# Kernel tuning notes

Measured on AMD Instinct MI355X. Metric: run time of the kernel, lower is better.

## Reference

```python
import jax, jax.numpy as jnp
import numpy as np


def setup_inputs() -> dict:
    key = jax.random.key(0)
    ks = jax.random.split(key, 5)
    S, B, I, H = 512, 64, 256, 1024
    scale_x = 1.0 / np.sqrt(I)
    scale_h = 1.0 / np.sqrt(H)
    return {
        "x": jax.random.normal(ks[0], (S, B, I), dtype=jnp.float32),
        "Wx": jax.random.normal(ks[1], (H, I), dtype=jnp.float32) * scale_x,
        "bx": jax.random.normal(ks[2], (H,), dtype=jnp.float32) * scale_x,
        "Wh": jax.random.normal(ks[3], (H, H), dtype=jnp.float32) * scale_h,
        "bh": jax.random.normal(ks[4], (H,), dtype=jnp.float32) * scale_h,
    }


def reference(x, Wx, bx, Wh, bh):
    # x: (S, B, I). Vanilla RNN: h_t = tanh(Wh h_{t-1} + bh + Wx x_t + bx)
    S, B, I = x.shape
    H = Wh.shape[0]
    # Precompute input projections for all timesteps in one big GEMM.
    xproj = jnp.einsum("sbi,hi->sbh", x, Wx) + bx  # (S, B, H)

    def step(h, xp_t):
        h_new = jnp.tanh(h @ Wh.T + bh + xp_t)  # (B, H)
        return h_new, h_new

    h0 = jnp.zeros((B, H), dtype=x.dtype)
    h_last, h_seq = jax.lax.scan(step, h0, xproj)
    return h_seq, h_last[None]  # (S,B,H), (1,B,H)
```

## Files before the change

kernel.cpp:

```cpp
#include <hip/hip_runtime.h>
#include <cstddef>

#define S_ 512
#define B_ 64
#define I_ 256
#define H_ 1024

#define NG 8
#define GB 8
#define JT 32
#define GBLK 32

__global__ __launch_bounds__(256) void transpose_k(const float* __restrict__ in,
                                                   float* __restrict__ out,
                                                   int R, int C) {
  __shared__ float t[32][33];
  int c0 = blockIdx.x * 32, r0 = blockIdx.y * 32;
  int x = threadIdx.x & 31, y = threadIdx.x >> 5;
  for (int i = 0; i < 32; i += 8) {
    t[y + i][x] = in[(size_t)(r0 + y + i) * C + (c0 + x)];
  }
  __syncthreads();
  for (int i = 0; i < 32; i += 8) {
    out[(size_t)(c0 + y + i) * R + (r0 + x)] = t[x][y + i];
  }
}

__global__ __launch_bounds__(256) void xproj_kernel(const float* __restrict__ x,
                                                    const float* __restrict__ WxT,
                                                    const float* __restrict__ bx,
                                                    float* __restrict__ out) {
  __shared__ float xs[8][I_];
  int tid = threadIdx.x;
  int j = blockIdx.x * 256 + tid;
  size_t m0 = (size_t)blockIdx.y * 8;
  const float* xrow = x + m0 * I_;
  #pragma unroll
  for (int r = 0; r < 8; ++r) xs[r][tid] = xrow[(size_t)r * I_ + tid];
  __syncthreads();

  float bj = bx[j];
  float a[8];
  #pragma unroll
  for (int r = 0; r < 8; ++r) a[r] = bj;
  const float* wp = WxT + j;
  for (int k = 0; k < I_; k += 4) {
    float w0 = wp[(size_t)(k + 0) * H_];
    float w1 = wp[(size_t)(k + 1) * H_];
    float w2 = wp[(size_t)(k + 2) * H_];
    float w3 = wp[(size_t)(k + 3) * H_];
    #pragma unroll
    for (int r = 0; r < 8; ++r) {
      float4 v = *(const float4*)&xs[r][k];
      a[r] += w0 * v.x + w1 * v.y + w2 * v.z + w3 * v.w;
    }
  }
  #pragma unroll
  for (int r = 0; r < 8; ++r) out[(m0 + r) * H_ + j] = a[r];
}

__global__ __launch_bounds__(512, 2) void rnn_persistent(
    const float* __restrict__ Wh, const float* __restrict__ bh,
    float* __restrict__ out, unsigned* __restrict__ flags) {
  __shared__ float4 Hs4[GB * 256];

  const int tid = threadIdx.x;
  const int g  = blockIdx.x & 7;
  const int jt = blockIdx.x >> 3;
  const int j0 = jt * JT, b0 = g * GB;
  const int jj = tid >> 4;
  const int ks = tid & 15;
  const int ksw = ks & 7;

  float4 Wreg[16];
  {
    const float4* wp = (const float4*)(Wh + (size_t)(j0 + jj) * H_) + ks * 16;
    #pragma unroll
    for (int i = 0; i < 16; ++i) Wreg[i] = wp[i];
  }
  const float bh_j = bh[j0 + jj];
  const size_t oidx = (size_t)(b0 + ksw) * H_ + (size_t)(j0 + jj);
  float* const out_last = out + (size_t)S_ * B_ * H_;
  unsigned* const flagg = flags + (size_t)g * GBLK;

  for (int t = 0; t < S_; ++t) {
    float* orow = out + (size_t)t * B_ * H_;
    float xv = orow[oidx];

    float s = 0.f;
    if (t > 0) {
      const float* hsrc =
          (const float*)(out + (size_t)(t - 1) * B_ * H_ + (size_t)b0 * H_);
      float4 hv[4];
      #pragma unroll
      for (int q = 0; q < 4; ++q) {
        const float* ap = hsrc + (size_t)(q * 512 + tid) * 4;
        asm volatile("global_load_dwordx4 %0, %1, off sc1"
                     : "=v"(hv[q]) : "v"(ap));
      }
      asm volatile("s_waitcnt vmcnt(0)" ::: "memory");
      __builtin_amdgcn_sched_barrier(0);
      #pragma unroll
      for (int q = 0; q < 4; ++q) {
        int f = q * 512 + tid;
        Hs4[f ^ ((f >> 4) & 7)] = hv[q];
      }
      __syncthreads();

      float acc[8] = {0.f, 0.f, 0.f, 0.f, 0.f, 0.f, 0.f, 0.f};
      const int kb = ks * 16;
      #pragma unroll
      for (int i = 0; i < 16; ++i) {
        const int l0 = kb + (i ^ ksw);
        const float4 w = Wreg[i];
        #pragma unroll
        for (int b = 0; b < 8; ++b) {
          float4 h = Hs4[b * 256 + l0];
          acc[b] += w.x * h.x + w.y * h.y + w.z * h.z + w.w * h.w;
        }
      }
      #pragma unroll
      for (int b = 0; b < 8; ++b) {
        float v = acc[b];
        v += __shfl_xor(v, 1, 64);
        v += __shfl_xor(v, 2, 64);
        v += __shfl_xor(v, 4, 64);
        v += __shfl_xor(v, 8, 64);
        acc[b] = v;
      }
      float sv = acc[0];
      #pragma unroll
      for (int b = 1; b < 8; ++b) sv = (ks == b) ? acc[b] : sv;
      s = sv;
    }

    if (ks < GB) {
      float hval = tanhf(s + bh_j + xv);
      if (t == S_ - 1) out_last[oidx] = hval;
      __hip_atomic_store(&orow[oidx], hval, __ATOMIC_RELAXED,
                         __HIP_MEMORY_SCOPE_AGENT);
    }

    if (t < S_ - 1) {
      asm volatile("s_waitcnt vmcnt(0)" ::: "memory");
      __syncthreads();
      if (tid == 0) {
        __hip_atomic_store(&flagg[jt], (unsigned)(t + 1), __ATOMIC_RELAXED,
                           __HIP_MEMORY_SCOPE_AGENT);
      }
      if (tid < 64) {
        unsigned* fp = &flagg[tid & 31];
        const unsigned tgt = (unsigned)(t + 1);
        while (__hip_atomic_load(fp, __ATOMIC_RELAXED,
                                 __HIP_MEMORY_SCOPE_AGENT) < tgt)
          __builtin_amdgcn_s_sleep(1);
      }
      __syncthreads();
    }
  }
}

extern "C" void kernel_launch(void* const* d_in, const int* in_sizes, int n_in,
                              void* d_out, int out_size, void* d_ws, size_t ws_size,
                              hipStream_t stream) {
  const float* x  = (const float*)d_in[0];
  const float* Wx = (const float*)d_in[1];
  const float* bx = (const float*)d_in[2];
  const float* Wh = (const float*)d_in[3];
  const float* bh = (const float*)d_in[4];
  float* out = (float*)d_out;
  float* WxT = (float*)d_ws;
  unsigned* flags = (unsigned*)(WxT + (size_t)I_ * H_);

  (void)hipMemsetAsync(flags, 0, NG * GBLK * sizeof(unsigned), stream);
  hipLaunchKernelGGL(transpose_k, dim3(I_ / 32, H_ / 32), dim3(256), 0, stream,
                     Wx, WxT, H_, I_);
  hipLaunchKernelGGL(xproj_kernel, dim3(H_ / 256, (S_ * B_) / 8), dim3(256), 0, stream,
                     x, WxT, bx, out);

  void* args[] = {(void*)&Wh, (void*)&bh, (void*)&out, (void*)&flags};
  hipError_t e = hipLaunchCooperativeKernel((const void*)rnn_persistent,
                                            dim3(256), dim3(512), args, 0, stream);
  if (e != hipSuccess) {
    hipLaunchKernelGGL(rnn_persistent, dim3(256), dim3(512), 0, stream,
                       Wh, bh, out, flags);
  }
}
```

Baseline: 4.300 ms.

## Interleave two batch groups per block to overlap barrier waits with compute

```diff
diff --git a/kernel.cpp b/kernel.cpp
--- a/kernel.cpp
+++ b/kernel.cpp
@@ -8,8 +8,8 @@
 
 #define NG 8
 #define GB 8
-#define JT 32
-#define GBLK 32
+#define JT 16
+#define GBLK 64
 
 __global__ __launch_bounds__(256) void transpose_k(const float* __restrict__ in,
                                                    float* __restrict__ out,
@@ -65,97 +65,177 @@
   __shared__ float4 Hs4[GB * 256];
 
   const int tid = threadIdx.x;
-  const int g  = blockIdx.x & 7;
-  const int jt = blockIdx.x >> 3;
-  const int j0 = jt * JT, b0 = g * GB;
-  const int jj = tid >> 4;
-  const int ks = tid & 15;
-  const int ksw = ks & 7;
-
-  float4 Wreg[16];
+  const int pr = blockIdx.x & 3;
+  const int jt = blockIdx.x >> 2;
+  const int j0 = jt * JT;
+  const int b0A = pr * GB, b0B = (pr + 4) * GB;
+  const int jj = tid >> 5;
+  const int ks = tid & 31;
+  const int hsw = (ks >> 1) & 7;
+
+  float4 Wreg[8];
   {
-    const float4* wp = (const float4*)(Wh + (size_t)(j0 + jj) * H_) + ks * 16;
+    const float4* wp = (const float4*)(Wh + (size_t)(j0 + jj) * H_) + ks * 8;
     #pragma unroll
-    for (int i = 0; i < 16; ++i) Wreg[i] = wp[i];
+    for (int i = 0; i < 8; ++i) {
+      const float4* ap = wp + i;
+      asm volatile("global_load_dwordx4 %0, %1, off" : "=v"(Wreg[i]) : "v"(ap));
+    }
+    asm volatile("s_waitcnt vmcnt(0)" ::: "memory");
+    __builtin_amdgcn_sched_barrier(0);
   }
   const float bh_j = bh[j0 + jj];
-  const size_t oidx = (size_t)(b0 + ksw) * H_ + (size_t)(j0 + jj);
+  const size_t oidxA = (size_t)(b0A + (ks & 7)) * H_ + (size_t)(j0 + jj);
+  const size_t oidxB = (size_t)(b0B + (ks & 7)) * H_ + (size_t)(j0 + jj);
   float* const out_last = out + (size_t)S_ * B_ * H_;
-  unsigned* const flagg = flags + (size_t)g * GBLK;
+  unsigned* const flagsA = flags + (size_t)pr * GBLK;
+  unsigned* const flagsB = flags + (size_t)(pr + 4) * GBLK;
 
   for (int t = 0; t < S_; ++t) {
     float* orow = out + (size_t)t * B_ * H_;
-    float xv = orow[oidx];
-
-    float s = 0.f;
-    if (t > 0) {
-      const float* hsrc =
-          (const float*)(out + (size_t)(t - 1) * B_ * H_ + (size_t)b0 * H_);
-      float4 hv[4];
-      #pragma unroll
-      for (int q = 0; q < 4; ++q) {
-        const float* ap = hsrc + (size_t)(q * 512 + tid) * 4;
-        asm volatile("global_load_dwordx4 %0, %1, off sc1"
-                     : "=v"(hv[q]) : "v"(ap));
-      }
-      asm volatile("s_waitcnt vmcnt(0)" ::: "memory");
-      __builtin_amdgcn_sched_barrier(0);
-      #pragma unroll
-      for (int q = 0; q < 4; ++q) {
-        int f = q * 512 + tid;
-        Hs4[f ^ ((f >> 4) & 7)] = hv[q];
-      }
-      __syncthreads();
-
-      float acc[8] = {0.f, 0.f, 0.f, 0.f, 0.f, 0.f, 0.f, 0.f};
-      const int kb = ks * 16;
-      #pragma unroll
-      for (int i = 0; i < 16; ++i) {
-        const int l0 = kb + (i ^ ksw);
-        const float4 w = Wreg[i];
+    float xvA = orow[oidxA];
+    float xvB = orow[oidxB];
+
+    {
+      float s = 0.f;
+      if (t > 0) {
+        if (tid < GBLK) {
+          unsigned* fp = &flagsA[tid];
+          while (__hip_atomic_load(fp, __ATOMIC_RELAXED,
+                                   __HIP_MEMORY_SCOPE_AGENT) < (unsigned)t)
+            __builtin_amdgcn_s_sleep(1);
+        }
+        __syncthreads();
+
+        const float* hsrc =
+            (const float*)(out + (size_t)(t - 1) * B_ * H_ + (size_t)b0A * H_);
+        float4 hv[4];
+        #pragma unroll
+        for (int q = 0; q < 4; ++q) {
+          const float* ap = hsrc + (size_t)(q * 512 + tid) * 4;
+          asm volatile("global_load_dwordx4 %0, %1, off sc1"
+                       : "=v"(hv[q]) : "v"(ap));
+        }
+        asm volatile("s_waitcnt vmcnt(0)" ::: "memory");
+        __builtin_amdgcn_sched_barrier(0);
+        #pragma unroll
+        for (int q = 0; q < 4; ++q) {
+          int f = q * 512 + tid;
+          Hs4[f ^ ((f >> 4) & 7)] = hv[q];
+        }
+        __syncthreads();
+
+        float acc[8] = {0.f, 0.f, 0.f, 0.f, 0.f, 0.f, 0.f, 0.f};
+        const int kb = ks * 8;
+        #pragma unroll
+        for (int i = 0; i < 8; ++i) {
+          const float4 w = Wreg[i];
+          const float4* hp = &Hs4[kb + (i ^ hsw)];
+          #pragma unroll
+          for (int b = 0; b < 8; ++b) {
+            float4 h = hp[b * 256];
+            acc[b] += w.x * h.x + w.y * h.y + w.z * h.z + w.w * h.w;
+          }
+        }
         #pragma unroll
         for (int b = 0; b < 8; ++b) {
-          float4 h = Hs4[b * 256 + l0];
-          acc[b] += w.x * h.x + w.y * h.y + w.z * h.z + w.w * h.w;
-        }
-      }
-      #pragma unroll
-      for (int b = 0; b < 8; ++b) {
-        float v = acc[b];
-        v += __shfl_xor(v, 1, 64);
-        v += __shfl_xor(v, 2, 64);
-        v += __shfl_xor(v, 4, 64);
-        v += __shfl_xor(v, 8, 64);
-        acc[b] = v;
-      }
-      float sv = acc[0];
-      #pragma unroll
-      for (int b = 1; b < 8; ++b) sv = (ks == b) ? acc[b] : sv;
-      s = sv;
-    }
-
-    if (ks < GB) {
-      float hval = tanhf(s + bh_j + xv);
-      if (t == S_ - 1) out_last[oidx] = hval;
-      __hip_atomic_store(&orow[oidx], hval, __ATOMIC_RELAXED,
-                         __HIP_MEMORY_SCOPE_AGENT);
-    }
-
-    if (t < S_ - 1) {
-      asm volatile("s_waitcnt vmcnt(0)" ::: "memory");
-      __syncthreads();
-      if (tid == 0) {
-        __hip_atomic_store(&flagg[jt], (unsigned)(t + 1), __ATOMIC_RELAXED,
+          float v = acc[b];
+          v += __shfl_xor(v, 1, 64);
+          v += __shfl_xor(v, 2, 64);
+          v += __shfl_xor(v, 4, 64);
+          v += __shfl_xor(v, 8, 64);
+          v += __shfl_xor(v, 16, 64);
+          acc[b] = v;
+        }
+        float sv = acc[0];
+        #pragma unroll
+        for (int b = 1; b < 8; ++b) sv = (ks == b) ? acc[b] : sv;
+        s = sv;
+      }
+      if (ks < GB) {
+        float hval = tanhf(s + bh_j + xvA);
+        if (t == S_ - 1) out_last[oidxA] = hval;
+        __hip_atomic_store(&orow[oidxA], hval, __ATOMIC_RELAXED,
                            __HIP_MEMORY_SCOPE_AGENT);
       }
-      if (tid < 64) {
-        unsigned* fp = &flagg[tid & 31];
-        const unsigned tgt = (unsigned)(t + 1);
-        while (__hip_atomic_load(fp, __ATOMIC_RELAXED,
-                                 __HIP_MEMORY_SCOPE_AGENT) < tgt)
-          __builtin_amdgcn_s_sleep(1);
-      }
-      __syncthreads();
+      if (t < S_ - 1) {
+        asm volatile("s_waitcnt vmcnt(0)" ::: "memory");
+        __syncthreads();
+        if (tid == 0)
+          __hip_atomic_store(&flagsA[jt], (unsigned)(t + 1), __ATOMIC_RELAXED,
+                             __HIP_MEMORY_SCOPE_AGENT);
+      }
+    }
+
+    {
+      float s = 0.f;
+      if (t > 0) {
+        if (tid < GBLK) {
+          unsigned* fp = &flagsB[tid];
+          while (__hip_atomic_load(fp, __ATOMIC_RELAXED,
+                                   __HIP_MEMORY_SCOPE_AGENT) < (unsigned)t)
+            __builtin_amdgcn_s_sleep(1);
+        }
+        __syncthreads();
+
+        const float* hsrc =
+            (const float*)(out + (size_t)(t - 1) * B_ * H_ + (size_t)b0B * H_);
+        float4 hv[4];
+        #pragma unroll
+        for (int q = 0; q < 4; ++q) {
+          const float* ap = hsrc + (size_t)(q * 512 + tid) * 4;
+          asm volatile("global_load_dwordx4 %0, %1, off sc1"
+                       : "=v"(hv[q]) : "v"(ap));
+        }
+        asm volatile("s_waitcnt vmcnt(0)" ::: "memory");
+        __builtin_amdgcn_sched_barrier(0);
+        #pragma unroll
+        for (int q = 0; q < 4; ++q) {
+          int f = q * 512 + tid;
+          Hs4[f ^ ((f >> 4) & 7)] = hv[q];
+        }
+        __syncthreads();
+
+        float acc[8] = {0.f, 0.f, 0.f, 0.f, 0.f, 0.f, 0.f, 0.f};
+        const int kb = ks * 8;
+        #pragma unroll
+        for (int i = 0; i < 8; ++i) {
+          const float4 w = Wreg[i];
+          const float4* hp = &Hs4[kb + (i ^ hsw)];
+          #pragma unroll
+          for (int b = 0; b < 8; ++b) {
+            float4 h = hp[b * 256];
+            acc[b] += w.x * h.x + w.y * h.y + w.z * h.z + w.w * h.w;
+          }
+        }
+        #pragma unroll
+        for (int b = 0; b < 8; ++b) {
+          float v = acc[b];
+          v += __shfl_xor(v, 1, 64);
+          v += __shfl_xor(v, 2, 64);
+          v += __shfl_xor(v, 4, 64);
+          v += __shfl_xor(v, 8, 64);
+          v += __shfl_xor(v, 16, 64);
+          acc[b] = v;
+        }
+        float sv = acc[0];
+        #pragma unroll
+        for (int b = 1; b < 8; ++b) sv = (ks == b) ? acc[b] : sv;
+        s = sv;
+      }
+      if (ks < GB) {
+        float hval = tanhf(s + bh_j + xvB);
+        if (t == S_ - 1) out_last[oidxB] = hval;
+        __hip_atomic_store(&orow[oidxB], hval, __ATOMIC_RELAXED,
+                           __HIP_MEMORY_SCOPE_AGENT);
+      }
+      if (t < S_ - 1) {
+        asm volatile("s_waitcnt vmcnt(0)" ::: "memory");
+        __syncthreads();
+        if (tid == 0)
+          __hip_atomic_store(&flagsB[jt], (unsigned)(t + 1), __ATOMIC_RELAXED,
+                             __HIP_MEMORY_SCOPE_AGENT);
+      }
     }
   }
 }
```

Measured after the change: 4.420 ms. +2.8%, slower.

## Split RNN recurrence across 512 smaller blocks with Wh streamed from cache

Applied to the files above, without the earlier changes.

```diff
diff --git a/kernel.cpp b/kernel.cpp
--- a/kernel.cpp
+++ b/kernel.cpp
@@ -8,8 +8,8 @@
 
 #define NG 8
 #define GB 8
-#define JT 32
-#define GBLK 32
+#define JT 16
+#define GBLK 64
 
 __global__ __launch_bounds__(256) void transpose_k(const float* __restrict__ in,
                                                    float* __restrict__ out,
@@ -59,27 +59,24 @@
   for (int r = 0; r < 8; ++r) out[(m0 + r) * H_ + j] = a[r];
 }
 
-__global__ __launch_bounds__(512, 2) void rnn_persistent(
+__global__ __launch_bounds__(256, 2) void rnn_persistent(
     const float* __restrict__ Wh, const float* __restrict__ bh,
     float* __restrict__ out, unsigned* __restrict__ flags) {
   __shared__ float4 Hs4[GB * 256];
 
   const int tid = threadIdx.x;
-  const int g  = blockIdx.x & 7;
-  const int jt = blockIdx.x >> 3;
+  const int g  = blockIdx.x >> 6;
+  const int jt = blockIdx.x & 63;
   const int j0 = jt * JT, b0 = g * GB;
-  const int jj = tid >> 4;
-  const int ks = tid & 15;
-  const int ksw = ks & 7;
+  const int b    = tid & 7;
+  const int half = (tid >> 3) & 1;
+  const int jj   = tid >> 4;
 
-  float4 Wreg[16];
-  {
-    const float4* wp = (const float4*)(Wh + (size_t)(j0 + jj) * H_) + ks * 16;
-    #pragma unroll
-    for (int i = 0; i < 16; ++i) Wreg[i] = wp[i];
-  }
   const float bh_j = bh[j0 + jj];
-  const size_t oidx = (size_t)(b0 + ksw) * H_ + (size_t)(j0 + jj);
+  const size_t oidx = (size_t)(b0 + b) * H_ + (size_t)(j0 + jj);
+  const float4* const wrow =
+      (const float4*)(Wh + (size_t)(j0 + jj) * H_ + (size_t)half * 512);
+  const int hbase = b * 256 + half * 128;
   float* const out_last = out + (size_t)S_ * B_ * H_;
   unsigned* const flagg = flags + (size_t)g * GBLK;
 
@@ -89,52 +86,53 @@
 
     float s = 0.f;
     if (t > 0) {
+      if (tid < GBLK) {
+        unsigned* fp = &flagg[tid];
+        while (__hip_atomic_load(fp, __ATOMIC_RELAXED,
+                                 __HIP_MEMORY_SCOPE_AGENT) < (unsigned)t)
+          __builtin_amdgcn_s_sleep(1);
+      }
+      __syncthreads();
+
       const float* hsrc =
           (const float*)(out + (size_t)(t - 1) * B_ * H_ + (size_t)b0 * H_);
-      float4 hv[4];
+      float4 hv[8];
       #pragma unroll
-      for (int q = 0; q < 4; ++q) {
-        const float* ap = hsrc + (size_t)(q * 512 + tid) * 4;
+      for (int q = 0; q < 8; ++q) {
+        const float* ap = hsrc + (size_t)(q * 256 + tid) * 4;
         asm volatile("global_load_dwordx4 %0, %1, off sc1"
                      : "=v"(hv[q]) : "v"(ap));
       }
       asm volatile("s_waitcnt vmcnt(0)" ::: "memory");
       __builtin_amdgcn_sched_barrier(0);
       #pragma unroll
-      for (int q = 0; q < 4; ++q) {
-        int f = q * 512 + tid;
-        Hs4[f ^ ((f >> 4) & 7)] = hv[q];
+      for (int q = 0; q < 8; ++q) {
+        Hs4[q * 256 + (tid ^ q)] = hv[q];
       }
       __syncthreads();
 
-      float acc[8] = {0.f, 0.f, 0.f, 0.f, 0.f, 0.f, 0.f, 0.f};
-      const int kb = ks * 16;
-      #pragma unroll
-      for (int i = 0; i < 16; ++i) {
-        const int l0 = kb + (i ^ ksw);
-        const float4 w = Wreg[i];
+      float4 accA = {0.f, 0.f, 0.f, 0.f};
+      float4 accB = {0.f, 0.f, 0.f, 0.f};
+      for (int k8 = 0; k8 < 128; k8 += 8) {
         #pragma unroll
-        for (int b = 0; b < 8; ++b) {
-          float4 h = Hs4[b * 256 + l0];
-          acc[b] += w.x * h.x + w.y * h.y + w.z * h.z + w.w * h.w;
+        for (int i = 0; i < 8; ++i) {
+          float4 w = wrow[k8 + i];
+          float4 h = Hs4[hbase + k8 + (i ^ b)];
+          if (i & 1) {
+            accB.x += w.x * h.x; accB.y += w.y * h.y;
+            accB.z += w.z * h.z; accB.w += w.w * h.w;
+          } else {
+            accA.x += w.x * h.x; accA.y += w.y * h.y;
+            accA.z += w.z * h.z; accA.w += w.w * h.w;
+          }
         }
       }
-      #pragma unroll
-      for (int b = 0; b < 8; ++b) {
-        float v = acc[b];
-        v += __shfl_xor(v, 1, 64);
-        v += __shfl_xor(v, 2, 64);
-        v += __shfl_xor(v, 4, 64);
-        v += __shfl_xor(v, 8, 64);
-        acc[b] = v;
-      }
-      float sv = acc[0];
-      #pragma unroll
-      for (int b = 1; b < 8; ++b) sv = (ks == b) ? acc[b] : sv;
-      s = sv;
+      float sum = ((accA.x + accA.y) + (accA.z + accA.w)) +
+                  ((accB.x + accB.y) + (accB.z + accB.w));
+      s = sum + __shfl_xor(sum, 8, 64);
     }
 
-    if (ks < GB) {
+    if (half == 0) {
       float hval = tanhf(s + bh_j + xv);
       if (t == S_ - 1) out_last[oidx] = hval;
       __hip_atomic_store(&orow[oidx], hval, __ATOMIC_RELAXED,
@@ -144,17 +142,9 @@
     if (t < S_ - 1) {
       asm volatile("s_waitcnt vmcnt(0)" ::: "memory");
       __syncthreads();
-      if (tid == 0) {
+      if (tid == 0)
         __hip_atomic_store(&flagg[jt], (unsigned)(t + 1), __ATOMIC_RELAXED,
                            __HIP_MEMORY_SCOPE_AGENT);
-      }
-      if (tid < 64) {
-        unsigned* fp = &flagg[tid & 31];
-        const unsigned tgt = (unsigned)(t + 1);
-        while (__hip_atomic_load(fp, __ATOMIC_RELAXED,
-                                 __HIP_MEMORY_SCOPE_AGENT) < tgt)
-          __builtin_amdgcn_s_sleep(1);
-      }
       __syncthreads();
     }
   }
@@ -180,9 +170,9 @@
 
   void* args[] = {(void*)&Wh, (void*)&bh, (void*)&out, (void*)&flags};
   hipError_t e = hipLaunchCooperativeKernel((const void*)rnn_persistent,
-                                            dim3(256), dim3(512), args, 0, stream);
+                                            dim3(512), dim3(256), args, 0, stream);
   if (e != hipSuccess) {
-    hipLaunchKernelGGL(rnn_persistent, dim3(256), dim3(512), 0, stream,
+    hipLaunchKernelGGL(rnn_persistent, dim3(512), dim3(256), 0, stream,
                        Wh, bh, out, flags);
   }
 }
```

Result: slower. 8.941 ms (+107.9%).
